# Performance work log

Measured on AMD Instinct MI355X. Metric: run time of the kernel, lower is better.

The kernel has to match this reference:

```python
import jax, jax.numpy as jnp
import numpy as np

QMAX = 7.0            # int4 narrow range: [-7, 7]
SCALING_MIN_VAL = 2e-16


def fake_quant_weight_per_channel(w):
    """Brevitas CommonIntWeightPerChannelQuant, bit_width=4.

    Per-output-channel float scale from abs-max stats, narrow-range signed
    int4 round+clamp, then dequantize. STE so gradients pass through.
    w: [O, I, KH, KW]
    """
    amax = jnp.max(jnp.abs(w), axis=(1, 2, 3), keepdims=True)   # [O,1,1,1]
    scale = jnp.maximum(amax / QMAX, SCALING_MIN_VAL)
    wq = jnp.clip(jnp.round(w / scale), -QMAX, QMAX) * scale
    # straight-through estimator (matches Brevitas round_ste backward)
    return w + jax.lax.stop_gradient(wq - w)


def setup_inputs() -> dict:
    key = jax.random.key(0)
    kx, kw = jax.random.split(key)
    x = jax.random.normal(kx, (32, 256, 56, 56), dtype=jnp.float32)
    # conv weight [out_channels, in_channels, kh, kw]
    w = jax.random.normal(kw, (256, 256, 3, 3), dtype=jnp.float32) * 0.05
    return {"x": x, "w": w}


def reference(x, w):
    wq = fake_quant_weight_per_channel(w)
    return jax.lax.conv_general_dilated(
        x, wq,
        window_strides=(1, 1),
        padding=((1, 1), (1, 1)),
        dimension_numbers=("NCHW", "OIHW", "NCHW"),
    )
```

## Files before the change

### kernel.cpp

```cpp
#include <hip/hip_runtime.h>
#include <cstdint>
#include <cstddef>

typedef __bf16 bf16x8 __attribute__((ext_vector_type(8)));
typedef float  f32x16 __attribute__((ext_vector_type(16)));
typedef int    i32x4  __attribute__((ext_vector_type(4)));

#define QMAX 7.0f
#define SCALE_MIN 2e-16f

#define BAR()     asm volatile("s_barrier" ::: "memory")
#define WAITVM(N) asm volatile("s_waitcnt vmcnt(" #N ")" ::: "memory")

__global__ __launch_bounds__(256) void quant_w_kernel(const float* __restrict__ w,
                                                      __bf16* __restrict__ wq) {
    const int o = blockIdx.x;
    const int t = threadIdx.x;
    const float* wo = w + (size_t)o * 2304;

    float vals[9];
    float m = 0.f;
    #pragma unroll
    for (int i = 0; i < 9; ++i) {
        float v = wo[t + i * 256];
        vals[i] = v;
        m = fmaxf(m, fabsf(v));
    }
    #pragma unroll
    for (int off = 32; off >= 1; off >>= 1) m = fmaxf(m, __shfl_down(m, off));
    __shared__ float red[4];
    __shared__ float s_scale;
    if ((t & 63) == 0) red[t >> 6] = m;
    __syncthreads();
    if (t == 0) {
        float am = fmaxf(fmaxf(red[0], red[1]), fmaxf(red[2], red[3]));
        s_scale = fmaxf(am / QMAX, SCALE_MIN);
    }
    __syncthreads();
    const float scale = s_scale;

    #pragma unroll
    for (int i = 0; i < 9; ++i) {
        int idx = t + i * 256;
        int c = idx / 9;
        int tap = idx - c * 9;
        float q = rintf(vals[i] / scale);
        q = fminf(QMAX, fmaxf(-QMAX, q));
        wq[(size_t)tap * 65536 + (size_t)o * 256 + c] = (__bf16)(q * scale);
    }
}

__global__ __launch_bounds__(256) void convert_x_kernel(const float* __restrict__ x,
                                                        __bf16* __restrict__ xpad) {
    __shared__ float tile[32][33];
    const int n  = blockIdx.z;
    const int c0 = blockIdx.y * 32;
    const int p0 = blockIdx.x * 32;
    const int tx = threadIdx.x & 31;
    const int ty = threadIdx.x >> 5;

    #pragma unroll
    for (int r = 0; r < 4; ++r) {
        int c = c0 + ty + r * 8;
        tile[ty + r * 8][tx] = x[((size_t)(n * 256 + c)) * 3136 + p0 + tx];
    }
    __syncthreads();
    #pragma unroll
    for (int r = 0; r < 4; ++r) {
        int p = p0 + ty + r * 8;
        int h = p / 56, wcol = p - h * 56;
        xpad[(((size_t)n * 58 + h + 1) * 58 + (wcol + 1)) * 256 + c0 + tx] =
            (__bf16)tile[tx][ty + r * 8];
    }
}

__global__ __launch_bounds__(256) void zero_halo_kernel(__bf16* __restrict__ xpad) {
    const int t = blockIdx.x * 256 + threadIdx.x;
    const int cvec = t & 31;
    const int r    = t >> 5;
    const int n    = r / 228;
    const int pos  = r - n * 228;
    if (n >= 32) return;
    int h, wcol;
    if      (pos < 58)  { h = 0;          wcol = pos; }
    else if (pos < 116) { h = 57;         wcol = pos - 58; }
    else if (pos < 172) { h = pos - 115;  wcol = 0; }
    else                { h = pos - 171;  wcol = 57; }
    i32x4* dst = (i32x4*)(xpad + (((size_t)n * 58 + h) * 58 + wcol) * 256);
    dst[cvec] = (i32x4){0, 0, 0, 0};
}

__device__ __forceinline__ void gload_lds16(const void* g, void* l) {
    __builtin_amdgcn_global_load_lds((const __attribute__((address_space(1))) void*)g,
                                     (__attribute__((address_space(3))) void*)l,
                                     16, 0, 0);
}

__global__ __launch_bounds__(256, 2) void conv_mfma_kernel(const __bf16* __restrict__ xpad,
                                                           const __bf16* __restrict__ wq,
                                                           float* __restrict__ out,
                                                           int* __restrict__ ticket) {
    extern __shared__ __align__(16) char lds[];
    int* s_t = (int*)(lds + 73728);
    const int tid  = threadIdx.x;
    const int wv   = tid >> 6;
    const int lane = tid & 63;

    const int wm = wv >> 1;
    const int wn = wv & 1;

    const int trow   = tid >> 2;
    const int schunk = (tid & 3) ^ ((tid >> 4) & 3);
    const __bf16* pA[4];
    #pragma unroll
    for (int j = 0; j < 4; ++j)
        pA[j] = wq + (size_t)(j * 64 + trow) * 256 + schunk * 8;
    const int adst = wv * 1024;
    const int bdst = 16384 + wv * 1024;

    const int l31 = lane & 31;
    const int lk  = lane >> 5;
    const int rsw = (lane >> 2) & 3;
    int kx[2];
    #pragma unroll
    for (int ks = 0; ks < 2; ++ks)
        kx[ks] = ((ks * 2 + lk) ^ rsw) * 16;
    int arow[4], brow[2];
    #pragma unroll
    for (int m = 0; m < 4; ++m) arow[m] = (wm * 128 + m * 32 + l31) * 64;
    #pragma unroll
    for (int n = 0; n < 2; ++n) brow[n] = 16384 + (wn * 64 + n * 32 + l31) * 64;
    const int hi = lane >> 5;

    for (;;) {
        __syncthreads();
        if (tid == 0) *s_t = atomicAdd(ticket, 1);
        __syncthreads();
        const int tile = *s_t;
        if (tile >= 784) break;
        const int p0 = tile * 128;

        const __bf16* pBs[2];
        #pragma unroll
        for (int j = 0; j < 2; ++j) {
            int pos = p0 + j * 64 + trow;
            int ni = pos / 3136;
            int hw = pos - ni * 3136;
            int h = hw / 56, w = hw - h * 56;
            pBs[j] = xpad + (((size_t)ni * 58 + h) * 58 + w) * 256 + schunk * 8;
        }

        f32x16 acc[4][2];
        #pragma unroll
        for (int m = 0; m < 4; ++m)
            #pragma unroll
            for (int n = 0; n < 2; ++n)
                acc[m][n] = (f32x16)(0.f);

        #define STAGE(STEP, BUF)                                                  \
            {                                                                     \
                const int tap_ = (STEP) >> 3, cc_ = (STEP) & 7;                   \
                const int kh_ = tap_ / 3, kw_ = tap_ - kh_ * 3;                   \
                const size_t aoff_ = (size_t)tap_ * 65536 + cc_ * 32;             \
                const size_t boff_ = (size_t)(kh_ * 58 + kw_) * 256 + cc_ * 32;   \
                gload_lds16(pA[0] + aoff_, (BUF) + adst);                         \
                gload_lds16(pA[1] + aoff_, (BUF) + adst + 4096);                  \
                gload_lds16(pA[2] + aoff_, (BUF) + adst + 8192);                  \
                gload_lds16(pA[3] + aoff_, (BUF) + adst + 12288);                 \
                gload_lds16(pBs[0] + boff_, (BUF) + bdst);                        \
                gload_lds16(pBs[1] + boff_, (BUF) + bdst + 4096);                 \
            }

        STAGE(0, lds);

        int co = 0;
        #pragma unroll 1
        for (int s = 0; s < 72; ++s) {
            int no = co + 24576; if (no == 73728) no = 0;
            if (s < 71) {
                STAGE(s + 1, lds + no);
                WAITVM(6);
            } else {
                WAITVM(0);
            }
            BAR();
            const char* B = lds + co;

            bf16x8 a0_[4], b0_[2];
            #pragma unroll
            for (int m = 0; m < 4; ++m)
                a0_[m] = *(const bf16x8*)(B + arow[m] + kx[0]);
            #pragma unroll
            for (int n = 0; n < 2; ++n)
                b0_[n] = *(const bf16x8*)(B + brow[n] + kx[0]);
            BAR();
            __builtin_amdgcn_s_setprio(1);
            #pragma unroll
            for (int m = 0; m < 4; ++m)
                #pragma unroll
                for (int n = 0; n < 2; ++n)
                    acc[m][n] = __builtin_amdgcn_mfma_f32_32x32x16_bf16(
                        a0_[m], b0_[n], acc[m][n], 0, 0, 0);
            __builtin_amdgcn_s_setprio(0);

            bf16x8 a1_[4], b1_[2];
            #pragma unroll
            for (int m = 0; m < 4; ++m)
                a1_[m] = *(const bf16x8*)(B + arow[m] + kx[1]);
            #pragma unroll
            for (int n = 0; n < 2; ++n)
                b1_[n] = *(const bf16x8*)(B + brow[n] + kx[1]);
            BAR();
            __builtin_amdgcn_s_setprio(1);
            #pragma unroll
            for (int m = 0; m < 4; ++m)
                #pragma unroll
                for (int n = 0; n < 2; ++n)
                    acc[m][n] = __builtin_amdgcn_mfma_f32_32x32x16_bf16(
                        a1_[m], b1_[n], acc[m][n], 0, 0, 0);
            __builtin_amdgcn_s_setprio(0);

            co = no;
        }
        #undef STAGE

        #pragma unroll
        for (int n = 0; n < 2; ++n) {
            const int pos = p0 + wn * 64 + n * 32 + l31;
            const int ni = pos / 3136;
            const int hw = pos - ni * 3136;
            float* ob = out + (size_t)ni * 802816 + hw;
            #pragma unroll
            for (int m = 0; m < 4; ++m) {
                const int om = wm * 128 + m * 32 + 4 * hi;
                #pragma unroll
                for (int r = 0; r < 16; ++r) {
                    const int o = om + (r & 3) + 8 * (r >> 2);
                    ob[(size_t)o * 3136] = acc[m][n][r];
                }
            }
        }
    }
}

__global__ __launch_bounds__(256) void conv_naive_kernel(const float* __restrict__ x,
                                                         const float* __restrict__ w,
                                                         float* __restrict__ out) {
    const int n = blockIdx.z;
    const int o = blockIdx.y;
    const int strip = blockIdx.x;
    __shared__ float wqs[2304];
    __shared__ float red[4];
    __shared__ float s_scale;
    const float* wo = w + (size_t)o * 2304;
    float m = 0.f;
    for (int i = threadIdx.x; i < 2304; i += 256) m = fmaxf(m, fabsf(wo[i]));
    #pragma unroll
    for (int off = 32; off >= 1; off >>= 1) m = fmaxf(m, __shfl_down(m, off));
    if ((threadIdx.x & 63) == 0) red[threadIdx.x >> 6] = m;
    __syncthreads();
    if (threadIdx.x == 0) {
        float am = fmaxf(fmaxf(red[0], red[1]), fmaxf(red[2], red[3]));
        s_scale = fmaxf(am / QMAX, SCALE_MIN);
    }
    __syncthreads();
    const float scale = s_scale;
    for (int i = threadIdx.x; i < 2304; i += 256) {
        float q = rintf(wo[i] / scale);
        q = fminf(QMAX, fmaxf(-QMAX, q));
        wqs[i] = q * scale;
    }
    __syncthreads();
    int p = strip * 256 + threadIdx.x;
    if (p >= 3136) return;
    int h = p / 56, wcol = p - h * 56;
    float acc = 0.f;
    for (int c = 0; c < 256; ++c) {
        const float* xc = x + ((size_t)(n * 256 + c)) * 3136;
        const float* wk = wqs + c * 9;
        #pragma unroll
        for (int kh = 0; kh < 3; ++kh) {
            int hh = h + kh - 1;
            if (hh < 0 || hh > 55) continue;
            #pragma unroll
            for (int kw = 0; kw < 3; ++kw) {
                int ww2 = wcol + kw - 1;
                if (ww2 < 0 || ww2 > 55) continue;
                acc += xc[hh * 56 + ww2] * wk[kh * 3 + kw];
            }
        }
    }
    out[((size_t)(n * 256 + o)) * 3136 + p] = acc;
}

extern "C" void kernel_launch(void* const* d_in, const int* in_sizes, int n_in,
                              void* d_out, int out_size, void* d_ws, size_t ws_size,
                              hipStream_t stream) {
    const float* x = (const float*)d_in[0];
    const float* w = (const float*)d_in[1];
    float* out = (float*)d_out;

    const size_t WQ_BYTES   = 9ull * 256 * 256 * 2;
    const size_t XPAD_OFF   = WQ_BYTES;
    const size_t XPAD_BYTES = 32ull * 58 * 58 * 256 * 2;
    const size_t TICKET_OFF = XPAD_OFF + XPAD_BYTES;

    if (ws_size >= TICKET_OFF + 64) {
        __bf16* wq   = (__bf16*)d_ws;
        __bf16* xpad = (__bf16*)((char*)d_ws + XPAD_OFF);
        int* ticket  = (int*)((char*)d_ws + TICKET_OFF);
        hipFuncSetAttribute((const void*)conv_mfma_kernel,
                            hipFuncAttributeMaxDynamicSharedMemorySize, 73792);
        hipMemsetAsync(ticket, 0, 4, stream);
        zero_halo_kernel<<<912, 256, 0, stream>>>(xpad);
        quant_w_kernel<<<256, 256, 0, stream>>>(w, wq);
        convert_x_kernel<<<dim3(98, 8, 32), 256, 0, stream>>>(x, xpad);
        conv_mfma_kernel<<<512, 256, 73792, stream>>>(xpad, wq, out, ticket);
    } else {
        conv_naive_kernel<<<dim3(13, 256, 32), 256, 0, stream>>>(x, w, out);
    }
}
```

Baseline: 182.7 us.

## Load weight tiles directly into registers and shrink LDS ring to activations only

The conv GEMM no longer stages weights through LDS. Each wave now owns 64 output channels and loads its A fragments straight from global memory into registers, double-buffered across steps. Only activation tiles go through a smaller three-slot LDS ring, and one of the per-step barriers is dropped. This cuts LDS traffic and footprint, which could allow more resident blocks. The cost is uncoalesced, latency-exposed global loads of weights and higher register pressure.

```diff
diff --git a/kernel.cpp b/kernel.cpp
--- a/kernel.cpp
+++ b/kernel.cpp
@@ -101,36 +101,27 @@
                                                            float* __restrict__ out,
                                                            int* __restrict__ ticket) {
     extern __shared__ __align__(16) char lds[];
-    int* s_t = (int*)(lds + 73728);
+    int* s_t = (int*)(lds + 24576);
     const int tid  = threadIdx.x;
     const int wv   = tid >> 6;
     const int lane = tid & 63;
-
-    const int wm = wv >> 1;
-    const int wn = wv & 1;
+    const int l31  = lane & 31;
+    const int hi   = lane >> 5;
+
+    const __bf16* pAr = wq + (size_t)(wv * 64 + l31) * 256 + hi * 8;
 
     const int trow   = tid >> 2;
     const int schunk = (tid & 3) ^ ((tid >> 4) & 3);
-    const __bf16* pA[4];
-    #pragma unroll
-    for (int j = 0; j < 4; ++j)
-        pA[j] = wq + (size_t)(j * 64 + trow) * 256 + schunk * 8;
-    const int adst = wv * 1024;
-    const int bdst = 16384 + wv * 1024;
-
-    const int l31 = lane & 31;
-    const int lk  = lane >> 5;
+    const int bdst   = wv * 1024;
+
     const int rsw = (lane >> 2) & 3;
     int kx[2];
     #pragma unroll
     for (int ks = 0; ks < 2; ++ks)
-        kx[ks] = ((ks * 2 + lk) ^ rsw) * 16;
-    int arow[4], brow[2];
-    #pragma unroll
-    for (int m = 0; m < 4; ++m) arow[m] = (wm * 128 + m * 32 + l31) * 64;
-    #pragma unroll
-    for (int n = 0; n < 2; ++n) brow[n] = 16384 + (wn * 64 + n * 32 + l31) * 64;
-    const int hi = lane >> 5;
+        kx[ks] = ((ks * 2 + hi) ^ rsw) * 16;
+    int brow[4];
+    #pragma unroll
+    for (int n = 0; n < 4; ++n) brow[n] = (n * 32 + l31) * 64;
 
     for (;;) {
         __syncthreads();
@@ -150,89 +141,88 @@
             pBs[j] = xpad + (((size_t)ni * 58 + h) * 58 + w) * 256 + schunk * 8;
         }
 
-        f32x16 acc[4][2];
+        f32x16 acc[2][4];
         #pragma unroll
-        for (int m = 0; m < 4; ++m)
+        for (int m = 0; m < 2; ++m)
             #pragma unroll
-            for (int n = 0; n < 2; ++n)
+            for (int n = 0; n < 4; ++n)
                 acc[m][n] = (f32x16)(0.f);
 
-        #define STAGE(STEP, BUF)                                                  \
-            {                                                                     \
-                const int tap_ = (STEP) >> 3, cc_ = (STEP) & 7;                   \
+        bf16x8 aA[2][2], aB[2][2];
+
+        {
+            gload_lds16(pBs[0], lds + bdst);
+            gload_lds16(pBs[1], lds + bdst + 4096);
+            aA[0][0] = *(const bf16x8*)(pAr);
+            aA[0][1] = *(const bf16x8*)(pAr + 16);
+            aA[1][0] = *(const bf16x8*)(pAr + 8192);
+            aA[1][1] = *(const bf16x8*)(pAr + 8192 + 16);
+        }
+
+        int co = 0;
+
+        #define STEPBODY(S, AC, AN)                                               \
+        {                                                                         \
+            const int s_ = (S);                                                   \
+            if (s_ < 71) {                                                        \
+                const int sn_ = s_ + 1;                                           \
+                const int tap_ = sn_ >> 3, cc_ = sn_ & 7;                         \
                 const int kh_ = tap_ / 3, kw_ = tap_ - kh_ * 3;                   \
+                const size_t boff_ = (size_t)(kh_ * 58 + kw_) * 256 + cc_ * 32;   \
                 const size_t aoff_ = (size_t)tap_ * 65536 + cc_ * 32;             \
-                const size_t boff_ = (size_t)(kh_ * 58 + kw_) * 256 + cc_ * 32;   \
-                gload_lds16(pA[0] + aoff_, (BUF) + adst);                         \
-                gload_lds16(pA[1] + aoff_, (BUF) + adst + 4096);                  \
-                gload_lds16(pA[2] + aoff_, (BUF) + adst + 8192);                  \
-                gload_lds16(pA[3] + aoff_, (BUF) + adst + 12288);                 \
-                gload_lds16(pBs[0] + boff_, (BUF) + bdst);                        \
-                gload_lds16(pBs[1] + boff_, (BUF) + bdst + 4096);                 \
-            }
-
-        STAGE(0, lds);
-
-        int co = 0;
+                int no_ = co + 8192; if (no_ == 24576) no_ = 0;                   \
+                gload_lds16(pBs[0] + boff_, lds + no_ + bdst);                    \
+                gload_lds16(pBs[1] + boff_, lds + no_ + bdst + 4096);             \
+                AN[0][0] = *(const bf16x8*)(pAr + aoff_);                         \
+                AN[0][1] = *(const bf16x8*)(pAr + aoff_ + 16);                    \
+                AN[1][0] = *(const bf16x8*)(pAr + aoff_ + 8192);                  \
+                AN[1][1] = *(const bf16x8*)(pAr + aoff_ + 8192 + 16);             \
+                WAITVM(6);                                                        \
+            } else { WAITVM(0); }                                                 \
+            BAR();                                                                \
+            const char* Bb = lds + co;                                            \
+            bf16x8 b_[4];                                                         \
+            _Pragma("unroll")                                                     \
+            for (int n = 0; n < 4; ++n)                                           \
+                b_[n] = *(const bf16x8*)(Bb + brow[n] + kx[0]);                   \
+            __builtin_amdgcn_s_setprio(1);                                        \
+            _Pragma("unroll")                                                     \
+            for (int m = 0; m < 2; ++m)                                           \
+                _Pragma("unroll")                                                 \
+                for (int n = 0; n < 4; ++n)                                       \
+                    acc[m][n] = __builtin_amdgcn_mfma_f32_32x32x16_bf16(          \
+                        AC[m][0], b_[n], acc[m][n], 0, 0, 0);                     \
+            __builtin_amdgcn_s_setprio(0);                                        \
+            _Pragma("unroll")                                                     \
+            for (int n = 0; n < 4; ++n)                                           \
+                b_[n] = *(const bf16x8*)(Bb + brow[n] + kx[1]);                   \
+            __builtin_amdgcn_s_setprio(1);                                        \
+            _Pragma("unroll")                                                     \
+            for (int m = 0; m < 2; ++m)                                           \
+                _Pragma("unroll")                                                 \
+                for (int n = 0; n < 4; ++n)                                       \
+                    acc[m][n] = __builtin_amdgcn_mfma_f32_32x32x16_bf16(          \
+                        AC[m][1], b_[n], acc[m][n], 0, 0, 0);                     \
+            __builtin_amdgcn_s_setprio(0);                                        \
+            co += 8192; if (co == 24576) co = 0;                                  \
+        }
+
         #pragma unroll 1
-        for (int s = 0; s < 72; ++s) {
-            int no = co + 24576; if (no == 73728) no = 0;
-            if (s < 71) {
-                STAGE(s + 1, lds + no);
-                WAITVM(6);
-            } else {
-                WAITVM(0);
-            }
-            BAR();
-            const char* B = lds + co;
-
-            bf16x8 a0_[4], b0_[2];
-            #pragma unroll
-            for (int m = 0; m < 4; ++m)
-                a0_[m] = *(const bf16x8*)(B + arow[m] + kx[0]);
-            #pragma unroll
-            for (int n = 0; n < 2; ++n)
-                b0_[n] = *(const bf16x8*)(B + brow[n] + kx[0]);
-            BAR();
-            __builtin_amdgcn_s_setprio(1);
-            #pragma unroll
-            for (int m = 0; m < 4; ++m)
-                #pragma unroll
-                for (int n = 0; n < 2; ++n)
-                    acc[m][n] = __builtin_amdgcn_mfma_f32_32x32x16_bf16(
-                        a0_[m], b0_[n], acc[m][n], 0, 0, 0);
-            __builtin_amdgcn_s_setprio(0);
-
-            bf16x8 a1_[4], b1_[2];
-            #pragma unroll
-            for (int m = 0; m < 4; ++m)
-                a1_[m] = *(const bf16x8*)(B + arow[m] + kx[1]);
-            #pragma unroll
-            for (int n = 0; n < 2; ++n)
-                b1_[n] = *(const bf16x8*)(B + brow[n] + kx[1]);
-            BAR();
-            __builtin_amdgcn_s_setprio(1);
-            #pragma unroll
-            for (int m = 0; m < 4; ++m)
-                #pragma unroll
-                for (int n = 0; n < 2; ++n)
-                    acc[m][n] = __builtin_amdgcn_mfma_f32_32x32x16_bf16(
-                        a1_[m], b1_[n], acc[m][n], 0, 0, 0);
-            __builtin_amdgcn_s_setprio(0);
-
-            co = no;
-        }
-        #undef STAGE
+        for (int i = 0; i < 36; ++i) {
+            STEPBODY(2 * i,     aA, aB);
+            STEPBODY(2 * i + 1, aB, aA);
+        }
+        #undef STEPBODY
 
         #pragma unroll
-        for (int n = 0; n < 2; ++n) {
-            const int pos = p0 + wn * 64 + n * 32 + l31;
+        for (int n = 0; n < 4; ++n) {
+            const int pos = p0 + n * 32 + l31;
             const int ni = pos / 3136;
             const int hw = pos - ni * 3136;
             float* ob = out + (size_t)ni * 802816 + hw;
             #pragma unroll
-            for (int m = 0; m < 4; ++m) {
-                const int om = wm * 128 + m * 32 + 4 * hi;
+            for (int m = 0; m < 2; ++m) {
+                const int om = wv * 64 + m * 32 + 4 * hi;
                 #pragma unroll
                 for (int r = 0; r < 16; ++r) {
                     const int o = om + (r & 3) + 8 * (r >> 2);
@@ -310,12 +300,12 @@
         __bf16* xpad = (__bf16*)((char*)d_ws + XPAD_OFF);
         int* ticket  = (int*)((char*)d_ws + TICKET_OFF);
         hipFuncSetAttribute((const void*)conv_mfma_kernel,
-                            hipFuncAttributeMaxDynamicSharedMemorySize, 73792);
+                            hipFuncAttributeMaxDynamicSharedMemorySize, 24640);
         hipMemsetAsync(ticket, 0, 4, stream);
         zero_halo_kernel<<<912, 256, 0, stream>>>(xpad);
         quant_w_kernel<<<256, 256, 0, stream>>>(w, wq);
         convert_x_kernel<<<dim3(98, 8, 32), 256, 0, stream>>>(x, xpad);
-        conv_mfma_kernel<<<512, 256, 73792, stream>>>(xpad, wq, out, ticket);
+        conv_mfma_kernel<<<512, 256, 24640, stream>>>(xpad, wq, out, ticket);
     } else {
         conv_naive_kernel<<<dim3(13, 256, 32), 256, 0, stream>>>(x, w, out);
     }
```

Measured after the change: 218.3 us. +19.5%, slower.
